# Performance work log

Measured on AMD Instinct MI355X. Metric: run time of the kernel, lower is better.

Reference implementation:

```python
import jax, jax.numpy as jnp
import numpy as np

C_IN = 64          # in_channel of DynamicFilter (conv2 of inter_prediction, hidden=64)
HID_DK = 32        # depth_kernel_mlp hidden width
C_GRP = C_IN + 4   # grouped feature channels: rel-xyz(3)+dist(1)+feat(C_IN)
MLP_H = 64         # mlp=[64, 64]


def _gather_nn(pts, idx):
    # pts: [B, N2, D], idx: [B, N, K] -> [B, N, K, D]
    B = pts.shape[0]
    return pts[jnp.arange(B)[:, None, None], idx]


def setup_inputs() -> dict:
    key = jax.random.key(0)
    ks = jax.random.split(key, 16)
    B, N, K = 1, 100000, 16
    xyz = jax.random.normal(ks[0], (B, N, 3), dtype=jnp.float32)
    xyz_nn = jax.random.normal(ks[1], (B, N, 3), dtype=jnp.float32)
    points = jax.random.normal(ks[2], (B, N, C_IN), dtype=jnp.float32)
    knn = jax.random.randint(ks[3], (B, N, K), 0, N)
    dists = jax.random.uniform(ks[4], (B, N, K), dtype=jnp.float32)
    mask = jax.random.uniform(ks[5], (B, N, K)) < 0.9  # ball-query mask (mostly in-ball)

    def lin(k, fan_in, fan_out):
        bound = 1.0 / np.sqrt(fan_in)
        kw, kb = jax.random.split(k)
        W = jax.random.uniform(kw, (fan_in, fan_out), minval=-bound, maxval=bound, dtype=jnp.float32)
        b = jax.random.uniform(kb, (fan_out,), minval=-bound, maxval=bound, dtype=jnp.float32)
        return W, b

    w_dk1, b_dk1 = lin(ks[6], C_GRP, HID_DK)
    w_dk2, b_dk2 = lin(ks[7], HID_DK, C_GRP)
    w_m1, b_m1 = lin(ks[8], C_GRP, MLP_H)
    w_m2, b_m2 = lin(ks[9], MLP_H, MLP_H)
    w_sc, b_sc = lin(ks[10], C_IN, MLP_H)
    return dict(xyz=xyz, xyz_nn=xyz_nn, points=points, knn=knn, dists=dists, mask=mask,
                w_dk1=w_dk1, b_dk1=b_dk1, w_dk2=w_dk2, b_dk2=b_dk2,
                w_m1=w_m1, b_m1=b_m1, w_m2=w_m2, b_m2=b_m2, w_sc=w_sc, b_sc=b_sc)


def reference(xyz, xyz_nn, points, knn, dists, mask,
              w_dk1, b_dk1, w_dk2, b_dk2, w_m1, b_m1, w_m2, b_m2, w_sc, b_sc):
    # --- grouping: relative neighbor coords + sqrt-dist + gathered features ---
    nn_xyz = _gather_nn(xyz_nn, knn)                                   # [B,N,K,3]
    grouped_xyz = jnp.concatenate(
        [nn_xyz - xyz[:, :, None, :], dists[..., None]], axis=-1)     # [B,N,K,4]
    grouped_points = jnp.concatenate(
        [grouped_xyz, _gather_nn(points, knn)], axis=-1)               # [B,N,K,4+C]

    # --- dynamic kernel MLP (per edge) ---
    h = jax.nn.relu(grouped_points @ w_dk1 + b_dk1)                    # [B,N,K,32]
    dk = h @ w_dk2 + b_dk2                                             # [B,N,K,4+C]

    # --- masked softmax over the K neighbor dim ---
    m = mask.astype(jnp.float32)[..., None]                            # [B,N,K,1]
    e = jnp.exp(dk - jnp.max(dk, axis=2, keepdims=True)) * m
    dk = e / (jnp.sum(e, axis=2, keepdims=True) + 1e-8)

    # --- weighted aggregation over neighbors ---
    agg = jnp.sum(dk * grouped_points, axis=2)                         # [B,N,4+C]

    # --- output MLP + residual shortcut ---
    out = jax.nn.relu(agg @ w_m1 + b_m1) @ w_m2 + b_m2                 # [B,N,64]
    out = points @ w_sc + b_sc + out
    return xyz, out
```

## Files before the change

kernel.cpp:

```cpp
#include <hip/hip_runtime.h>
#include <cstdint>


namespace {

typedef _Float16 half8  __attribute__((ext_vector_type(8)));
typedef _Float16 half4v __attribute__((ext_vector_type(4)));
typedef _Float16 half2v __attribute__((ext_vector_type(2)));
typedef float    f32x4  __attribute__((ext_vector_type(4)));

template <int I> struct IC { static constexpr int value = I; };

constexpr int K   = 16;
constexpr int CIN = 64;
constexpr int CG  = 68;
constexpr int HID = 32;
constexpr int MH  = 64;

constexpr int X_LD   = 104;
constexpr int AGG_LD = 96;
constexpr int PTS    = 8;
constexpr float LOG2E = 1.44269504f;

constexpr int FW1_SZ = 64 * 48;
constexpr int FW2_SZ = 64 * 40;
constexpr int FB_SZ  = 64 * 16;
constexpr int FTAB_SZ = FW1_SZ + FW2_SZ + FB_SZ;

__device__ inline bool mask_is_int32(const void* m) {
    const uint32_t* p = (const uint32_t*)m;
    uint32_t acc = 0;
    #pragma unroll
    for (int i = 0; i < 16; ++i) acc |= p[i] & 0xFFFFFF00u;
    return acc == 0;
}

__device__ inline void lgkm_fence() {
    asm volatile("s_waitcnt lgkmcnt(0)" ::: "memory");
}

__device__ inline half2v pk2h(float a, float b) {
    return __builtin_bit_cast(half2v, __builtin_amdgcn_cvt_pkrtz(a, b));
}

__global__ __launch_bounds__(256) void cvt_kernel(
    const float* __restrict__ in, _Float16* __restrict__ out, int n4)
{
    for (int i = blockIdx.x * 256 + threadIdx.x; i < n4; i += gridDim.x * 256) {
        const float4 v = ((const float4*)in)[i];
        half4v h = { (_Float16)v.x, (_Float16)v.y, (_Float16)v.z, (_Float16)v.w };
        ((half4v*)out)[i] = h;
    }
}

__global__ __launch_bounds__(512) void prep_kernel(
    const float* __restrict__ w1, const float* __restrict__ b1,
    const float* __restrict__ w2, const float* __restrict__ b2,
    _Float16* __restrict__ ftab)
{
    const int tid = threadIdx.x;
    for (int i = tid; i < FW1_SZ; i += 512) {
        const int ln = i / 48, j = i % 48;
        const int hb = j / 24, kc = (j % 24) / 8, e = j % 8;
        const int mm = ln & 15, gg = ln >> 4;
        const int col = kc * 32 + gg * 8 + e;
        float v = 0.f;
        if (col < 64)      v = w1[(4 + col) * HID + hb * 16 + mm];
        else if (col < 68) v = w1[(col - 64) * HID + hb * 16 + mm];
        ftab[i] = (_Float16)v;
    }
    for (int i = tid; i < FW2_SZ; i += 512) {
        const int ln = i / 40, j = i % 40;
        const int nt = j / 8, e = j % 8;
        const int mm = ln & 15, gg = ln >> 4;
        const int sig = (e < 4) ? gg * 4 + e : 16 + gg * 4 + (e - 4);
        const int oc  = nt * 16 + mm;
        ftab[FW1_SZ + i] = (oc < CG) ? (_Float16)(w2[sig * CG + oc] * LOG2E)
                                     : (_Float16)0.f;
    }
    for (int i = tid; i < FB_SZ; i += 512) {
        const int ln = i / 16, j = i % 16;
        const int mm = ln & 15, gg = ln >> 4;
        float v = 0.f;
        if (j < 4)       v = b1[gg * 4 + j];
        else if (j < 8)  v = b1[16 + gg * 4 + (j - 4)];
        else if (j < 13) {
            const int nt = j - 8;
            v = (((nt * 16 + mm < CG) ? b2[nt * 16 + mm] : 0.f) - 2.0f) * LOG2E;
        }
        ftab[FW1_SZ + FW2_SZ + i] = (_Float16)v;
    }
}

__global__ __launch_bounds__(512, 4) void edge_kernel(
    const float* __restrict__ xyz, const float* __restrict__ xyz_nn,
    const _Float16* __restrict__ pts16, const int* __restrict__ knn,
    const float* __restrict__ dists, const void* __restrict__ mask,
    const _Float16* __restrict__ ftab,
    _Float16* __restrict__ aggw, int N)
{
    __shared__ __align__(16) _Float16 sXt[8][5 * 256];
    __shared__ __align__(16) _Float16 sFrag[FW1_SZ + FW2_SZ];
    __shared__ __align__(16) _Float16 sFB[FB_SZ];
    __shared__ __align__(16) int      sPIdx[8][PTS][16];
    __shared__ __align__(16) _Float16 sPMk[8][PTS][16];
    __shared__ __align__(16) _Float16 sPD[8][PTS][16];
    __shared__ __align__(16) float    sPXyz[8][PTS][4];

    const int tid  = threadIdx.x;
    const int w    = tid >> 6;
    const int lane = tid & 63;
    const int m    = lane & 15;
    const int g    = lane >> 4;

    const bool is32 = mask_is_int32(mask);

    {
        const half8* __restrict__ ft8 = (const half8*)ftab;
        half8* __restrict__ fr8 = (half8*)sFrag;
        #pragma unroll 2
        for (int i = tid; i < (FW1_SZ + FW2_SZ) / 8; i += 512)
            fr8[i] = ft8[i];
        half8* __restrict__ fb8 = (half8*)sFB;
        for (int i = tid; i < FB_SZ / 8; i += 512)
            fb8[i] = ft8[(FW1_SZ + FW2_SZ) / 8 + i];
    }

    const int pbase = blockIdx.x * (8 * PTS);
    for (int i = tid; i < 8 * PTS * 16; i += 512) {
        const int gi = min(pbase * 16 + i, N * 16 - 1);
        ((int*)sPIdx)[i] = knn[gi];
        const int mv = is32 ? ((const int*)mask)[gi]
                            : (int)((const uint8_t*)mask)[gi];
        ((_Float16*)sPMk)[i] = mv ? (_Float16)1.f : (_Float16)0.f;
        ((_Float16*)sPD)[i]  = (_Float16)dists[gi];
    }
    for (int i = tid; i < 8 * PTS * 4; i += 512) {
        const int pt = i >> 2, c = i & 3;
        const int gp_ = min(pbase + pt, N - 1);
        ((float*)sPXyz)[i] = (c < 3) ? xyz[gp_ * 3 + c] : 0.f;
    }

    char* const XwB = (char*)&sXt[w][0];
    if (lane < 16) {
        half4v z = {};
        *(half4v*)(XwB + 4 * 512 + lane * 32 + 8)  = z;
        *(half4v*)(XwB + 4 * 512 + lane * 32 + 16) = z;
        *(half4v*)(XwB + 4 * 512 + lane * 32 + 24) = z;
    }
    __syncthreads();

    half8 W1A[2][3];
    #pragma unroll
    for (int hb = 0; hb < 2; ++hb)
        #pragma unroll
        for (int kc = 0; kc < 3; ++kc)
            W1A[hb][kc] = *(const half8*)&sFrag[lane * 48 + (hb * 3 + kc) * 8];
    half8 W2B[5];
    #pragma unroll
    for (int nt = 0; nt < 5; ++nt)
        W2B[nt] = *(const half8*)&sFrag[FW1_SZ + lane * 40 + nt * 8];
    float b1v[4], b1w[4], b2v[5];
    {
        half4v bA = *(const half4v*)&sFB[lane * 16];
        half4v bB = *(const half4v*)&sFB[lane * 16 + 4];
        #pragma unroll
        for (int r = 0; r < 4; ++r) { b1v[r] = (float)bA[r]; b1w[r] = (float)bB[r]; }
        #pragma unroll
        for (int nt = 0; nt < 5; ++nt) b2v[nt] = (float)sFB[lane * 16 + 8 + nt];
    }
    const half4v ones = { (_Float16)1.f, (_Float16)1.f,
                          (_Float16)1.f, (_Float16)1.f };

    auto tadr = [&](int c) -> char* {
        return XwB + ((c >> 4) * 512 + m * 32 + (c & 15) * 2);
    };
    half4v* const wF0lo = (half4v*)tadr(4 + 8 * g);
    half4v* const wF0hi = (half4v*)tadr(8 + 8 * g);
    half4v* const wF1lo = (half4v*)tadr(36 + 8 * g);
    half4v* const wF1hi = (half4v*)tadr(40 + 8 * g);
    half4v* const wGeo  = (half4v*)tadr(0);
    const uint32_t xrd = (uint32_t)(uintptr_t)XwB + lane * 8;

    const int nbase = (blockIdx.x * 8 + w) * PTS;

    float stNx[2], stNy[2], stNz[2];
    half8 stF0[2], stF1[2];

    auto issueB = [&](int pp, auto bfc) {
        constexpr int bf = decltype(bfc)::value;
        const int idx = sPIdx[w][pp][m];
        stF0[bf] = *(const half8*)&pts16[(size_t)idx * CIN + g * 8];
        stF1[bf] = *(const half8*)&pts16[(size_t)idx * CIN + 32 + g * 8];
        if (g == 0) {
            stNx[bf] = xyz_nn[idx * 3 + 0];
            stNy[bf] = xyz_nn[idx * 3 + 1];
            stNz[bf] = xyz_nn[idx * 3 + 2];
        }
    };

    auto body = [&](int p, auto curc, auto nxtc) {
        constexpr int buf = decltype(curc)::value;
        const bool val = (nbase + p < N);
        const int n = val ? nbase + p : 0;

        half4v mk4 = *(const half4v*)&sPMk[w][p][g * 4];
        const half2v mk01 = { mk4[0], mk4[1] };
        const half2v mk23 = { mk4[2], mk4[3] };
        half8 geoF = {};
        if (g == 0) {
            const float cx = sPXyz[w][p][0];
            const float cy = sPXyz[w][p][1];
            const float cz = sPXyz[w][p][2];
            geoF[0] = (_Float16)(stNx[buf] - cx);
            geoF[1] = (_Float16)(stNy[buf] - cy);
            geoF[2] = (_Float16)(stNz[buf] - cz);
            geoF[3] = sPD[w][p][m];
        }

        half4v f0lo, f0hi, f1lo, f1hi;
        #pragma unroll
        for (int j = 0; j < 4; ++j) {
            f0lo[j] = stF0[buf][j]; f0hi[j] = stF0[buf][4 + j];
            f1lo[j] = stF1[buf][j]; f1hi[j] = stF1[buf][4 + j];
        }
        *wF0lo = f0lo; *wF0hi = f0hi; *wF1lo = f1lo; *wF1hi = f1hi;
        if (g == 0) {
            half4v gv = { geoF[0], geoF[1], geoF[2], geoF[3] };
            *wGeo = gv;
        }
        lgkm_fence();

        half4v xq0, xq1, xq2, xq3, xq4;
        asm volatile(
            "ds_read_b64_tr_b16 %0, %5\n\t"
            "ds_read_b64_tr_b16 %1, %5 offset:512\n\t"
            "ds_read_b64_tr_b16 %2, %5 offset:1024\n\t"
            "ds_read_b64_tr_b16 %3, %5 offset:1536\n\t"
            "ds_read_b64_tr_b16 %4, %5 offset:2048"
            : "=&v"(xq0), "=&v"(xq1), "=&v"(xq2), "=&v"(xq3), "=&v"(xq4)
            : "v"(xrd));

        issueB(p + 1 < PTS ? p + 1 : PTS - 1, nxtc);

        f32x4 a0 = {0.f, 0.f, 0.f, 0.f};
        f32x4 a1 = {0.f, 0.f, 0.f, 0.f};
        a0 = __builtin_amdgcn_mfma_f32_16x16x32_f16(W1A[0][0], stF0[buf], a0, 0, 0, 0);
        a1 = __builtin_amdgcn_mfma_f32_16x16x32_f16(W1A[1][0], stF0[buf], a1, 0, 0, 0);
        a0 = __builtin_amdgcn_mfma_f32_16x16x32_f16(W1A[0][1], stF1[buf], a0, 0, 0, 0);
        a1 = __builtin_amdgcn_mfma_f32_16x16x32_f16(W1A[1][1], stF1[buf], a1, 0, 0, 0);
        a0 = __builtin_amdgcn_mfma_f32_16x16x32_f16(W1A[0][2], geoF,      a0, 0, 0, 0);
        a1 = __builtin_amdgcn_mfma_f32_16x16x32_f16(W1A[1][2], geoF,      a1, 0, 0, 0);

        half8 A2;
        #pragma unroll
        for (int r = 0; r < 4; ++r) {
            A2[r]     = (_Float16)fmaxf(a0[r] + b1v[r], 0.f);
            A2[4 + r] = (_Float16)fmaxf(a1[r] + b1w[r], 0.f);
        }

        asm volatile("s_waitcnt lgkmcnt(0)" ::: "memory");
        __builtin_amdgcn_sched_barrier(0);

        const half4v xqs[5] = { xq0, xq1, xq2, xq3, xq4 };
        const size_t obase = (size_t)n * AGG_LD;

        #pragma unroll
        for (int nt = 0; nt < 5; ++nt) {
            f32x4 acc = {0.f, 0.f, 0.f, 0.f};
            acc = __builtin_amdgcn_mfma_f32_16x16x32_f16(A2, W2B[nt], acc, 0, 0, 0);
            const float bb = b2v[nt];
            half2v ef01 = pk2h(__builtin_amdgcn_exp2f(acc[0] + bb),
                               __builtin_amdgcn_exp2f(acc[1] + bb)) * mk01;
            half2v ef23 = pk2h(__builtin_amdgcn_exp2f(acc[2] + bb),
                               __builtin_amdgcn_exp2f(acc[3] + bb)) * mk23;
            const half2v xlo = { xqs[nt][0], xqs[nt][1] };
            const half2v xhi = { xqs[nt][2], xqs[nt][3] };
            const half2v exf01 = ef01 * xlo;
            const half2v exf23 = ef23 * xhi;
            const half4v ef  = { ef01[0], ef01[1], ef23[0], ef23[1] };
            const half4v exf = { exf01[0], exf01[1], exf23[0], exf23[1] };
            f32x4 sden = {0.f, 0.f, 0.f, 0.f};
            f32x4 snum = {0.f, 0.f, 0.f, 0.f};
            sden = __builtin_amdgcn_mfma_f32_16x16x16f16(ones, ef,  sden, 0, 0, 0);
            snum = __builtin_amdgcn_mfma_f32_16x16x16f16(ones, exf, snum, 0, 0, 0);
            const float aggv = snum[0] * __builtin_amdgcn_rcpf(sden[0] + 1e-8f);
            if (val && g == (nt & 3)) aggw[obase + nt * 16 + m] = (_Float16)aggv;
        }
        if (val && lane < 16) aggw[obase + 80 + lane] = (_Float16)0.f;
    };

    issueB(0, IC<0>{});
    #pragma unroll
    for (int p = 0; p < PTS; p += 2) {
        body(p,     IC<0>{}, IC<1>{});
        body(p + 1, IC<1>{}, IC<0>{});
    }
}

__global__ __launch_bounds__(512) void point_kernel(
    const float* __restrict__ xyz, const _Float16* __restrict__ pts16,
    const _Float16* __restrict__ aggw,
    const float* __restrict__ wm1, const float* __restrict__ bm1,
    const float* __restrict__ wm2, const float* __restrict__ bm2,
    const float* __restrict__ wsc, const float* __restrict__ bsc,
    float* __restrict__ out, int N, int ntiles)
{
    __shared__ __align__(16) _Float16 sWm1[64 * X_LD];
    __shared__ __align__(16) _Float16 sWm2[64 * 72];
    __shared__ __align__(16) _Float16 sWsc[64 * 72];
    __shared__ float sBm1[64], sB2c[64];
    __shared__ __align__(16) _Float16 sH2[8][16 * 72];

    const int tid = threadIdx.x;

    for (int gid = blockIdx.x * 512 + tid; gid < 3 * N; gid += gridDim.x * 512)
        out[gid] = xyz[gid];

    for (int i = tid; i < 64 * X_LD; i += 512) {
        const int c = i / X_LD, k = i % X_LD;
        sWm1[i] = (k < CG) ? (_Float16)wm1[k * MH + c] : (_Float16)0.f;
    }
    for (int i = tid; i < 64 * 72; i += 512) {
        const int c = i / 72, k = i % 72;
        sWm2[i] = (k < MH) ? (_Float16)wm2[k * MH + c] : (_Float16)0.f;
        sWsc[i] = (k < MH) ? (_Float16)wsc[k * MH + c] : (_Float16)0.f;
    }
    if (tid < 64) { sBm1[tid] = bm1[tid]; sB2c[tid] = bm2[tid] + bsc[tid]; }
    __syncthreads();

    const int w = tid >> 6, lane = tid & 63;
    const int m = lane & 15, g = lane >> 4;
    const int t = blockIdx.x * 8 + w;
    if (t >= ntiles) return;
    const int row0 = t * 16;
    _Float16* __restrict__ H2 = sH2[w];

    const int rl = min(row0 + m, N - 1);

    f32x4 acc[4] = {{0.f,0.f,0.f,0.f},{0.f,0.f,0.f,0.f},
                    {0.f,0.f,0.f,0.f},{0.f,0.f,0.f,0.f}};
    #pragma unroll
    for (int kc = 0; kc < 3; ++kc) {
        const int ko = kc * 32 + g * 8;
        half8 a = *(const half8*)&aggw[(size_t)rl * AGG_LD + ko];
        #pragma unroll
        for (int nt = 0; nt < 4; ++nt) {
            half8 b = *(const half8*)&sWm1[(nt * 16 + m) * X_LD + ko];
            acc[nt] = __builtin_amdgcn_mfma_f32_16x16x32_f16(a, b, acc[nt], 0, 0, 0);
        }
    }
    #pragma unroll
    for (int nt = 0; nt < 4; ++nt) {
        const float bb = sBm1[nt * 16 + m];
        #pragma unroll
        for (int r = 0; r < 4; ++r)
            H2[(g * 4 + r) * 72 + nt * 16 + m] = (_Float16)fmaxf(acc[nt][r] + bb, 0.f);
    }
    lgkm_fence();

    f32x4 acc2[4] = {{0.f,0.f,0.f,0.f},{0.f,0.f,0.f,0.f},
                     {0.f,0.f,0.f,0.f},{0.f,0.f,0.f,0.f}};
    #pragma unroll
    for (int kc = 0; kc < 2; ++kc) {
        const int ko = kc * 32 + g * 8;
        half8 ah = *(const half8*)&H2[m * 72 + ko];
        half8 ap = *(const half8*)&pts16[(size_t)rl * CIN + ko];
        #pragma unroll
        for (int nt = 0; nt < 4; ++nt) {
            half8 b2f = *(const half8*)&sWm2[(nt * 16 + m) * 72 + ko];
            half8 bsf = *(const half8*)&sWsc[(nt * 16 + m) * 72 + ko];
            acc2[nt] = __builtin_amdgcn_mfma_f32_16x16x32_f16(ah, b2f, acc2[nt], 0, 0, 0);
            acc2[nt] = __builtin_amdgcn_mfma_f32_16x16x32_f16(ap, bsf, acc2[nt], 0, 0, 0);
        }
    }
    float* __restrict__ outp = out + (size_t)3 * N;
    #pragma unroll
    for (int nt = 0; nt < 4; ++nt) {
        const float bb = sB2c[nt * 16 + m];
        #pragma unroll
        for (int r = 0; r < 4; ++r) {
            const int row = row0 + g * 4 + r;
            if (row < N) outp[(size_t)row * MH + nt * 16 + m] = acc2[nt][r] + bb;
        }
    }
}

__global__ __launch_bounds__(256) void fused_ip_kernel(
    const float* __restrict__ xyz, const float* __restrict__ xyz_nn,
    const float* __restrict__ points, const int* __restrict__ knn,
    const float* __restrict__ dists, const void* __restrict__ mask,
    const float* __restrict__ w1, const float* __restrict__ b1,
    const float* __restrict__ w2, const float* __restrict__ b2,
    const float* __restrict__ wm1, const float* __restrict__ bm1,
    const float* __restrict__ wm2, const float* __restrict__ bm2,
    const float* __restrict__ wsc, const float* __restrict__ bsc,
    float* __restrict__ out, int N)
{
    __shared__ __align__(16) float gp[4][K][72];
    __shared__ float hb [4][K][33];
    __shared__ float dkb[4][K][69];
    __shared__ float mkb[4][K];
    __shared__ int   sidx[4][K];
    __shared__ float aggb[4][CG];
    __shared__ float h2b[4][MH];
    __shared__ float ptb[4][CIN];

    const int tid  = threadIdx.x;
    const int w    = tid >> 6;
    const int lane = tid & 63;
    {
        int gid = blockIdx.x * 256 + tid;
        if (gid < 3 * N) out[gid] = xyz[gid];
    }
    int n = blockIdx.x * 4 + w;
    const bool valid = (n < N);
    if (!valid) n = 0;
    float* __restrict__ outp = out + (size_t)3 * N;

    if (lane < K) {
        const int idx = knn[n * K + lane];
        sidx[w][lane] = idx;
        const bool mv = mask_is_int32(mask)
            ? (((const int*)mask)[n * K + lane] != 0)
            : (((const uint8_t*)mask)[n * K + lane] != 0);
        mkb[w][lane]  = mv ? 1.0f : 0.0f;
        const float cx = xyz[n * 3 + 0], cy = xyz[n * 3 + 1], cz = xyz[n * 3 + 2];
        gp[w][lane][0] = xyz_nn[idx * 3 + 0] - cx;
        gp[w][lane][1] = xyz_nn[idx * 3 + 1] - cy;
        gp[w][lane][2] = xyz_nn[idx * 3 + 2] - cz;
        gp[w][lane][3] = dists[n * K + lane];
    }
    ptb[w][lane] = points[(size_t)n * CIN + lane];
    __syncthreads();
    for (int k = 0; k < K; ++k) {
        const int idx = sidx[w][k];
        gp[w][k][4 + lane] = points[(size_t)idx * CIN + lane];
    }
    __syncthreads();
    {
        const int j  = lane & 31;
        const int kh = lane >> 5;
        float acc[8];
        const float bj = b1[j];
        #pragma unroll
        for (int kk = 0; kk < 8; ++kk) acc[kk] = bj;
        for (int c4 = 0; c4 < 17; ++c4) {
            float w1v[4];
            #pragma unroll
            for (int i = 0; i < 4; ++i) w1v[i] = w1[(c4 * 4 + i) * HID + j];
            #pragma unroll
            for (int kk = 0; kk < 8; ++kk) {
                const int k = kk * 2 + kh;
                const float4 g4 = *reinterpret_cast<const float4*>(&gp[w][k][c4 * 4]);
                acc[kk] += g4.x * w1v[0] + g4.y * w1v[1] + g4.z * w1v[2] + g4.w * w1v[3];
            }
        }
        #pragma unroll
        for (int kk = 0; kk < 8; ++kk) {
            const int k = kk * 2 + kh;
            hb[w][k][j] = fmaxf(acc[kk], 0.0f);
        }
    }
    __syncthreads();
    {
        const int k = lane >> 2;
        const int q = lane & 3;
        float acc[17];
        #pragma unroll
        for (int i = 0; i < 17; ++i) acc[i] = b2[q * 17 + i];
        for (int j2 = 0; j2 < HID; ++j2) {
            const float hv = hb[w][k][j2];
            const float* __restrict__ w2r = &w2[j2 * CG + q * 17];
            #pragma unroll
            for (int i = 0; i < 17; ++i) acc[i] += hv * w2r[i];
        }
        #pragma unroll
        for (int i = 0; i < 17; ++i) dkb[w][k][q * 17 + i] = acc[i];
    }
    __syncthreads();
    {
        #pragma unroll
        for (int rep = 0; rep < 2; ++rep) {
            const int c = rep * 64 + lane;
            if (c < CG) {
                float v[K];
                float mm = -1e30f;
                #pragma unroll
                for (int k = 0; k < K; ++k) { v[k] = dkb[w][k][c]; mm = fmaxf(mm, v[k]); }
                float s = 0.0f;
                #pragma unroll
                for (int k = 0; k < K; ++k) {
                    const float e = __expf(v[k] - mm) * mkb[w][k];
                    v[k] = e; s += e;
                }
                const float inv = 1.0f / (s + 1e-8f);
                float a = 0.0f;
                #pragma unroll
                for (int k = 0; k < K; ++k) a += v[k] * gp[w][k][c];
                aggb[w][c] = a * inv;
            }
        }
    }
    __syncthreads();
    {
        float acc = bm1[lane];
        for (int c = 0; c < CG; ++c) acc += aggb[w][c] * wm1[c * MH + lane];
        h2b[w][lane] = fmaxf(acc, 0.0f);
    }
    __syncthreads();
    {
        float acc = bm2[lane] + bsc[lane];
        for (int j2 = 0; j2 < MH; ++j2) acc += h2b[w][j2] * wm2[j2 * MH + lane];
        for (int c = 0; c < CIN; ++c)  acc += ptb[w][c] * wsc[c * MH + lane];
        if (valid) outp[(size_t)n * MH + lane] = acc;
    }
}

}

extern "C" void kernel_launch(void* const* d_in, const int* in_sizes, int n_in,
                              void* d_out, int out_size, void* d_ws, size_t ws_size,
                              hipStream_t stream)
{
    const float*   xyz    = (const float*)d_in[0];
    const float*   xyz_nn = (const float*)d_in[1];
    const float*   points = (const float*)d_in[2];
    const int*     knn    = (const int*)d_in[3];
    const float*   dists  = (const float*)d_in[4];
    const void*    mask   = d_in[5];
    const float*   w1  = (const float*)d_in[6];
    const float*   b1  = (const float*)d_in[7];
    const float*   w2  = (const float*)d_in[8];
    const float*   b2  = (const float*)d_in[9];
    const float*   wm1 = (const float*)d_in[10];
    const float*   bm1 = (const float*)d_in[11];
    const float*   wm2 = (const float*)d_in[12];
    const float*   bm2 = (const float*)d_in[13];
    const float*   wsc = (const float*)d_in[14];
    const float*   bsc = (const float*)d_in[15];

    float* out = (float*)d_out;
    const int N = in_sizes[0] / 3;
    const size_t agg_bytes = (size_t)N * AGG_LD * sizeof(_Float16);
    const size_t pts_bytes = (size_t)N * CIN * sizeof(_Float16);
    const size_t ftab_bytes = (size_t)FTAB_SZ * sizeof(_Float16);

    if (ws_size >= agg_bytes + pts_bytes + ftab_bytes) {
        _Float16* aggw  = (_Float16*)d_ws;
        _Float16* pts16 = (_Float16*)((char*)d_ws + agg_bytes);
        _Float16* ftab  = (_Float16*)((char*)d_ws + agg_bytes + pts_bytes);

        hipLaunchKernelGGL(cvt_kernel, dim3(2048), dim3(256), 0, stream,
                           points, pts16, N * CIN / 4);
        hipLaunchKernelGGL(prep_kernel, dim3(1), dim3(512), 0, stream,
                           w1, b1, w2, b2, ftab);

        const int ppb     = 8 * PTS;
        const int blocks1 = (N + ppb - 1) / ppb;
        hipLaunchKernelGGL(edge_kernel, dim3(blocks1), dim3(512), 0, stream,
                           xyz, xyz_nn, pts16, knn, dists, mask,
                           ftab, aggw, N);

        const int ntiles  = (N + 15) / 16;
        const int blocks2 = (ntiles + 7) / 8;
        hipLaunchKernelGGL(point_kernel, dim3(blocks2), dim3(512), 0, stream,
                           xyz, pts16, aggw, wm1, bm1, wm2, bm2, wsc, bsc,
                           out, N, ntiles);
    } else {
        const int blocks = (N + 3) / 4;
        hipLaunchKernelGGL(fused_ip_kernel, dim3(blocks), dim3(256), 0, stream,
                           xyz, xyz_nn, points, knn, dists, mask,
                           w1, b1, w2, b2, wm1, bm1, wm2, bm2, wsc, bsc,
                           out, N);
    }
}
```

Measured before the change: 112.5 us.

## Fold weight prep into convert kernel and pre-pack point-kernel weights

Drops the separate prep_kernel launch by doing the edge-weight fragment packing in block 0 of the convert kernel. Block 1 now also pre-transposes and converts the output-MLP and shortcut weights to fp16 into a workspace table, so every point_kernel block copies them with vector loads instead of doing per-block scalar transpose and convert. The edge kernel's launch bound is raised from 4 to 6 waves per SIMD, which limits registers per thread and risks spills. Biases are now stored in fp16, which slightly lowers precision.

```diff
diff --git a/kernel.cpp b/kernel.cpp
--- a/kernel.cpp
+++ b/kernel.cpp
@@ -27,6 +27,12 @@
 constexpr int FB_SZ  = 64 * 16;
 constexpr int FTAB_SZ = FW1_SZ + FW2_SZ + FB_SZ;
 
+constexpr int PW1_OFF = 0;
+constexpr int PW2_OFF = 64 * X_LD;
+constexpr int PSC_OFF = PW2_OFF + 64 * 72;
+constexpr int PB_OFF  = PSC_OFF + 64 * 72;
+constexpr int PTAB_SZ = PB_OFF + 128;
+
 __device__ inline bool mask_is_int32(const void* m) {
     const uint32_t* p = (const uint32_t*)m;
     uint32_t acc = 0;
@@ -44,55 +50,72 @@
 }
 
 __global__ __launch_bounds__(256) void cvt_kernel(
-    const float* __restrict__ in, _Float16* __restrict__ out, int n4)
+    const float* __restrict__ in, _Float16* __restrict__ out, int n4,
+    const float* __restrict__ w1, const float* __restrict__ b1,
+    const float* __restrict__ w2, const float* __restrict__ b2,
+    const float* __restrict__ wm1, const float* __restrict__ bm1,
+    const float* __restrict__ wm2, const float* __restrict__ bm2,
+    const float* __restrict__ wsc, const float* __restrict__ bsc,
+    _Float16* __restrict__ ftab, _Float16* __restrict__ ptab)
 {
-    for (int i = blockIdx.x * 256 + threadIdx.x; i < n4; i += gridDim.x * 256) {
+    const int tid = threadIdx.x;
+    if (blockIdx.x == 0) {
+        for (int i = tid; i < FW1_SZ; i += 256) {
+            const int ln = i / 48, j = i % 48;
+            const int hb = j / 24, kc = (j % 24) / 8, e = j % 8;
+            const int mm = ln & 15, gg = ln >> 4;
+            const int col = kc * 32 + gg * 8 + e;
+            float v = 0.f;
+            if (col < 64)      v = w1[(4 + col) * HID + hb * 16 + mm];
+            else if (col < 68) v = w1[(col - 64) * HID + hb * 16 + mm];
+            ftab[i] = (_Float16)v;
+        }
+        for (int i = tid; i < FW2_SZ; i += 256) {
+            const int ln = i / 40, j = i % 40;
+            const int nt = j / 8, e = j % 8;
+            const int mm = ln & 15, gg = ln >> 4;
+            const int sig = (e < 4) ? gg * 4 + e : 16 + gg * 4 + (e - 4);
+            const int oc  = nt * 16 + mm;
+            ftab[FW1_SZ + i] = (oc < CG) ? (_Float16)(w2[sig * CG + oc] * LOG2E)
+                                         : (_Float16)0.f;
+        }
+        for (int i = tid; i < FB_SZ; i += 256) {
+            const int ln = i / 16, j = i % 16;
+            const int mm = ln & 15, gg = ln >> 4;
+            float v = 0.f;
+            if (j < 4)       v = b1[gg * 4 + j];
+            else if (j < 8)  v = b1[16 + gg * 4 + (j - 4)];
+            else if (j < 13) {
+                const int nt = j - 8;
+                v = (((nt * 16 + mm < CG) ? b2[nt * 16 + mm] : 0.f) - 2.0f) * LOG2E;
+            }
+            ftab[FW1_SZ + FW2_SZ + i] = (_Float16)v;
+        }
+    } else if (blockIdx.x == 1) {
+        for (int i = tid; i < 64 * X_LD; i += 256) {
+            const int c = i / X_LD, k = i % X_LD;
+            ptab[PW1_OFF + i] = (k < CG) ? (_Float16)wm1[k * MH + c]
+                                         : (_Float16)0.f;
+        }
+        for (int i = tid; i < 64 * 72; i += 256) {
+            const int c = i / 72, k = i % 72;
+            ptab[PW2_OFF + i] = (k < MH) ? (_Float16)wm2[k * MH + c]
+                                         : (_Float16)0.f;
+            ptab[PSC_OFF + i] = (k < MH) ? (_Float16)wsc[k * MH + c]
+                                         : (_Float16)0.f;
+        }
+        for (int i = tid; i < 128; i += 256)
+            ptab[PB_OFF + i] = (i < 64) ? (_Float16)bm1[i]
+                                        : (_Float16)(bm2[i - 64] + bsc[i - 64]);
+    }
+    for (int i = blockIdx.x * 256 + tid; i < n4; i += gridDim.x * 256) {
         const float4 v = ((const float4*)in)[i];
         half4v h = { (_Float16)v.x, (_Float16)v.y, (_Float16)v.z, (_Float16)v.w };
         ((half4v*)out)[i] = h;
     }
 }
 
-__global__ __launch_bounds__(512) void prep_kernel(
-    const float* __restrict__ w1, const float* __restrict__ b1,
-    const float* __restrict__ w2, const float* __restrict__ b2,
-    _Float16* __restrict__ ftab)
-{
-    const int tid = threadIdx.x;
-    for (int i = tid; i < FW1_SZ; i += 512) {
-        const int ln = i / 48, j = i % 48;
-        const int hb = j / 24, kc = (j % 24) / 8, e = j % 8;
-        const int mm = ln & 15, gg = ln >> 4;
-        const int col = kc * 32 + gg * 8 + e;
-        float v = 0.f;
-        if (col < 64)      v = w1[(4 + col) * HID + hb * 16 + mm];
-        else if (col < 68) v = w1[(col - 64) * HID + hb * 16 + mm];
-        ftab[i] = (_Float16)v;
-    }
-    for (int i = tid; i < FW2_SZ; i += 512) {
-        const int ln = i / 40, j = i % 40;
-        const int nt = j / 8, e = j % 8;
-        const int mm = ln & 15, gg = ln >> 4;
-        const int sig = (e < 4) ? gg * 4 + e : 16 + gg * 4 + (e - 4);
-        const int oc  = nt * 16 + mm;
-        ftab[FW1_SZ + i] = (oc < CG) ? (_Float16)(w2[sig * CG + oc] * LOG2E)
-                                     : (_Float16)0.f;
-    }
-    for (int i = tid; i < FB_SZ; i += 512) {
-        const int ln = i / 16, j = i % 16;
-        const int mm = ln & 15, gg = ln >> 4;
-        float v = 0.f;
-        if (j < 4)       v = b1[gg * 4 + j];
-        else if (j < 8)  v = b1[16 + gg * 4 + (j - 4)];
-        else if (j < 13) {
-            const int nt = j - 8;
-            v = (((nt * 16 + mm < CG) ? b2[nt * 16 + mm] : 0.f) - 2.0f) * LOG2E;
-        }
-        ftab[FW1_SZ + FW2_SZ + i] = (_Float16)v;
-    }
-}
-
-__global__ __launch_bounds__(512, 4) void edge_kernel(
+__global__ __launch_bounds__(512, 6) void edge_kernel(
     const float* __restrict__ xyz, const float* __restrict__ xyz_nn,
     const _Float16* __restrict__ pts16, const int* __restrict__ knn,
     const float* __restrict__ dists, const void* __restrict__ mask,
@@ -300,16 +323,10 @@
 
 __global__ __launch_bounds__(512) void point_kernel(
     const float* __restrict__ xyz, const _Float16* __restrict__ pts16,
-    const _Float16* __restrict__ aggw,
-    const float* __restrict__ wm1, const float* __restrict__ bm1,
-    const float* __restrict__ wm2, const float* __restrict__ bm2,
-    const float* __restrict__ wsc, const float* __restrict__ bsc,
+    const _Float16* __restrict__ aggw, const _Float16* __restrict__ ptab,
     float* __restrict__ out, int N, int ntiles)
 {
-    __shared__ __align__(16) _Float16 sWm1[64 * X_LD];
-    __shared__ __align__(16) _Float16 sWm2[64 * 72];
-    __shared__ __align__(16) _Float16 sWsc[64 * 72];
-    __shared__ float sBm1[64], sB2c[64];
+    __shared__ __align__(16) _Float16 sW[PTAB_SZ];
     __shared__ __align__(16) _Float16 sH2[8][16 * 72];
 
     const int tid = threadIdx.x;
@@ -317,17 +334,18 @@
     for (int gid = blockIdx.x * 512 + tid; gid < 3 * N; gid += gridDim.x * 512)
         out[gid] = xyz[gid];
 
-    for (int i = tid; i < 64 * X_LD; i += 512) {
-        const int c = i / X_LD, k = i % X_LD;
-        sWm1[i] = (k < CG) ? (_Float16)wm1[k * MH + c] : (_Float16)0.f;
-    }
-    for (int i = tid; i < 64 * 72; i += 512) {
-        const int c = i / 72, k = i % 72;
-        sWm2[i] = (k < MH) ? (_Float16)wm2[k * MH + c] : (_Float16)0.f;
-        sWsc[i] = (k < MH) ? (_Float16)wsc[k * MH + c] : (_Float16)0.f;
-    }
-    if (tid < 64) { sBm1[tid] = bm1[tid]; sB2c[tid] = bm2[tid] + bsc[tid]; }
-    __syncthreads();
+    {
+        const half8* __restrict__ pt8 = (const half8*)ptab;
+        half8* __restrict__ sw8 = (half8*)sW;
+        #pragma unroll 4
+        for (int i = tid; i < PTAB_SZ / 8; i += 512)
+            sw8[i] = pt8[i];
+    }
+    __syncthreads();
+
+    const _Float16* __restrict__ sWm1 = &sW[PW1_OFF];
+    const _Float16* __restrict__ sWm2 = &sW[PW2_OFF];
+    const _Float16* __restrict__ sWsc = &sW[PSC_OFF];
 
     const int w = tid >> 6, lane = tid & 63;
     const int m = lane & 15, g = lane >> 4;
@@ -352,7 +370,7 @@
     }
     #pragma unroll
     for (int nt = 0; nt < 4; ++nt) {
-        const float bb = sBm1[nt * 16 + m];
+        const float bb = (float)sW[PB_OFF + nt * 16 + m];
         #pragma unroll
         for (int r = 0; r < 4; ++r)
             H2[(g * 4 + r) * 72 + nt * 16 + m] = (_Float16)fmaxf(acc[nt][r] + bb, 0.f);
@@ -377,7 +395,7 @@
     float* __restrict__ outp = out + (size_t)3 * N;
     #pragma unroll
     for (int nt = 0; nt < 4; ++nt) {
-        const float bb = sB2c[nt * 16 + m];
+        const float bb = (float)sW[PB_OFF + 64 + nt * 16 + m];
         #pragma unroll
         for (int r = 0; r < 4; ++r) {
             const int row = row0 + g * 4 + r;
@@ -542,19 +560,21 @@
 
     float* out = (float*)d_out;
     const int N = in_sizes[0] / 3;
-    const size_t agg_bytes = (size_t)N * AGG_LD * sizeof(_Float16);
-    const size_t pts_bytes = (size_t)N * CIN * sizeof(_Float16);
+    const size_t agg_bytes  = (size_t)N * AGG_LD * sizeof(_Float16);
+    const size_t pts_bytes  = (size_t)N * CIN * sizeof(_Float16);
     const size_t ftab_bytes = (size_t)FTAB_SZ * sizeof(_Float16);
-
-    if (ws_size >= agg_bytes + pts_bytes + ftab_bytes) {
+    const size_t ptab_bytes = (size_t)PTAB_SZ * sizeof(_Float16);
+
+    if (ws_size >= agg_bytes + pts_bytes + ftab_bytes + ptab_bytes) {
         _Float16* aggw  = (_Float16*)d_ws;
         _Float16* pts16 = (_Float16*)((char*)d_ws + agg_bytes);
         _Float16* ftab  = (_Float16*)((char*)d_ws + agg_bytes + pts_bytes);
+        _Float16* ptab  = (_Float16*)((char*)d_ws + agg_bytes + pts_bytes + ftab_bytes);
 
         hipLaunchKernelGGL(cvt_kernel, dim3(2048), dim3(256), 0, stream,
-                           points, pts16, N * CIN / 4);
-        hipLaunchKernelGGL(prep_kernel, dim3(1), dim3(512), 0, stream,
-                           w1, b1, w2, b2, ftab);
+                           points, pts16, N * CIN / 4,
+                           w1, b1, w2, b2, wm1, bm1, wm2, bm2, wsc, bsc,
+                           ftab, ptab);
 
         const int ppb     = 8 * PTS;
         const int blocks1 = (N + ppb - 1) / ppb;
@@ -565,8 +585,7 @@
         const int ntiles  = (N + 15) / 16;
         const int blocks2 = (ntiles + 7) / 8;
         hipLaunchKernelGGL(point_kernel, dim3(blocks2), dim3(512), 0, stream,
-                           xyz, pts16, aggw, wm1, bm1, wm2, bm2, wsc, bsc,
-                           out, N, ntiles);
+                           xyz, pts16, aggw, ptab, out, N, ntiles);
     } else {
         const int blocks = (N + 3) / 4;
         hipLaunchKernelGGL(fused_ip_kernel, dim3(blocks), dim3(256), 0, stream,
```

After: 265.7 us. 136% more time.
